# Optimization experiments

Hardware: AMD Instinct MI355X
Metric: run time of the kernel (lower is better)

The kernel has to match this reference:

```python
import jax, jax.numpy as jnp
import numpy as np

EMBD_SIZE = 128
NUM_HEADS = 8
HEAD_SIZE = 16

def setup_inputs() -> dict:
    key = jax.random.key(0)
    ks = jax.random.split(key, 6)
    B, S = 8, 2048
    x = jax.random.normal(ks[0], (B, S, EMBD_SIZE), dtype=jnp.float32)
    # per-head Linear weights, torch layout [out, in] stacked over heads -> [H, hs, E]
    sc = 1.0 / np.sqrt(EMBD_SIZE)
    Wk = jax.random.normal(ks[1], (NUM_HEADS, HEAD_SIZE, EMBD_SIZE), dtype=jnp.float32) * sc
    Wq = jax.random.normal(ks[2], (NUM_HEADS, HEAD_SIZE, EMBD_SIZE), dtype=jnp.float32) * sc
    Wv = jax.random.normal(ks[3], (NUM_HEADS, HEAD_SIZE, EMBD_SIZE), dtype=jnp.float32) * sc
    Wp = jax.random.normal(ks[4], (EMBD_SIZE, NUM_HEADS * HEAD_SIZE), dtype=jnp.float32) * sc
    bp = jax.random.normal(ks[5], (EMBD_SIZE,), dtype=jnp.float32) * 0.01
    return {"x": x, "Wk": Wk, "Wq": Wq, "Wv": Wv, "Wp": Wp, "bp": bp}

def reference(x, Wk, Wq, Wv, Wp, bp):
    # x: [B,S,E]; W{k,q,v}: [H,hs,E]; Wp: [E,H*hs]
    B, S, E = x.shape
    H, hs, _ = Wk.shape
    q = jnp.einsum('bse,hde->bhsd', x, Wq)
    k = jnp.einsum('bse,hde->bhsd', x, Wk)
    v = jnp.einsum('bse,hde->bhsd', x, Wv)
    # NOTE: original code MULTIPLIES by sqrt(head_size) (k.shape[-1]**0.5)
    scores = jnp.einsum('bhsd,bhtd->bhst', q, k) * (hs ** 0.5)
    wei = jax.nn.softmax(scores, axis=-1)  # dropout is identity in eval mode
    out = jnp.einsum('bhst,bhtd->bhsd', wei, v)
    # concat heads along last dim: [B,S,H*hs]
    out = out.transpose(0, 2, 1, 3).reshape(B, S, H * hs)
    return out @ Wp.T + bp
```

## Files before the change

### kernel.cpp

```cpp
#include <hip/hip_runtime.h>
#include <hip/hip_bf16.h>

constexpr int Bb  = 8;
constexpr int Ss  = 2048;
constexpr int Ee  = 128;
constexpr int Hh  = 8;
constexpr int HSs = 16;
constexpr int QKVSZ = Bb * Hh * Ss * HSs;

typedef _Float16 f16;
typedef __attribute__((ext_vector_type(8)))  _Float16 f16x8;
typedef __attribute__((ext_vector_type(16))) float f32x16;

constexpr float QSCALE = 5.770780163555854f;

__device__ __forceinline__ unsigned pack_rtz(float lo, float hi) {
    union { __fp16 __attribute__((ext_vector_type(2))) h; unsigned u; } c;
    c.h = __builtin_amdgcn_cvt_pkrtz(lo, hi);
    return c.u;
}
__device__ __forceinline__ unsigned pack_rne(float lo, float hi) {
    union { __attribute__((ext_vector_type(2))) _Float16 h; unsigned u; } c;
    c.h[0] = (f16)lo; c.h[1] = (f16)hi;
    return c.u;
}

__global__ __launch_bounds__(256) void prep_w(
    const float* __restrict__ Wq, const float* __restrict__ Wk,
    const float* __restrict__ Wv, const float* __restrict__ Wp,
    f16* __restrict__ wh)
{
    int i = (blockIdx.x * 256 + threadIdx.x) * 4;
    const float* src = (i < 16384) ? (Wq + i)
                     : (i < 32768) ? (Wk + i - 16384)
                     : (i < 49152) ? (Wv + i - 32768) : (Wp + i - 49152);
    float4 v = *(const float4*)src;
    union { f16 h[4]; uint2 u; } c;
    c.h[0] = (f16)v.x; c.h[1] = (f16)v.y; c.h[2] = (f16)v.z; c.h[3] = (f16)v.w;
    *(uint2*)(wh + i) = c.u;
}

__global__ __launch_bounds__(256) void qkv_kernel(
    const float* __restrict__ x, const f16* __restrict__ wh,
    f16* __restrict__ qo, f16* __restrict__ ko, f16* __restrict__ vo)
{
    constexpr int LDW = 136;
    __shared__ __align__(16) f16 Xs[32 * LDW];

    const int mat = blockIdx.y;
    const int rowbase = blockIdx.x * 32;

    for (int idx = threadIdx.x; idx < 32 * 32; idx += 256) {
        const int r = idx >> 5, cp = idx & 31;
        float4 v = *(const float4*)(x + (size_t)(rowbase + r) * Ee + cp * 4);
        union { f16 h[4]; uint2 u; } c;
        c.h[0] = (f16)v.x; c.h[1] = (f16)v.y; c.h[2] = (f16)v.z; c.h[3] = (f16)v.w;
        *(uint2*)&Xs[r * LDW + cp * 4] = c.u;
    }
    __syncthreads();

    const int wv_ = threadIdx.x >> 6, lane = threadIdx.x & 63;
    const int h = lane >> 5, n31 = lane & 31;

    f16x8 A[8];
#pragma unroll
    for (int t = 0; t < 8; ++t)
        A[t] = *(const f16x8*)&Xs[n31 * LDW + 16 * t + 8 * h];
    __syncthreads();

    const int c = wv_ * 32 + n31;
    const f16* wr = wh + mat * 16384 + (size_t)c * Ee + 8 * h;
    f32x16 acc = {};
#pragma unroll
    for (int t = 0; t < 8; ++t)
        acc = __builtin_amdgcn_mfma_f32_32x32x16_f16(A[t], *(const f16x8*)(wr + 16 * t), acc, 0, 0, 0);

    const float scale = (mat == 1) ? QSCALE : 1.f;
#pragma unroll
    for (int r = 0; r < 16; ++r) {
        const int row = (r & 3) + 8 * (r >> 2) + 4 * h;
        Xs[row * LDW + c] = (f16)(acc[r] * scale);
    }
    __syncthreads();

    f16* dst = (mat == 0) ? qo : ((mat == 1) ? ko : vo);
    const int b = rowbase >> 11;
    const int s0 = rowbase & 2047;
    if (mat < 2) {
        for (int i = threadIdx.x; i < 512; i += 256) {
            const int head = i >> 6, rem = i & 63;
            const int s = rem >> 1, dh = rem & 1;
            const int bh = b * Hh + head;
            *(uint4*)(dst + ((size_t)bh * Ss + s0 + s) * HSs + dh * 8) =
                *(const uint4*)&Xs[s * LDW + head * HSs + dh * 8];
        }
    } else {
        for (int i = threadIdx.x; i < 512; i += 256) {
            const int head = i >> 6, rem = i & 63;
            const int d = rem & 15, ehalf = (rem >> 4) & 1, squart = rem >> 5;
            const int bh = b * Hh + head;
            union { f16 hv[8]; uint4 u; } pkt;
#pragma unroll
            for (int j = 0; j < 8; ++j) {
                const int ls = squart * 16 + ehalf * 8 + j;
                pkt.hv[j] = Xs[ls * LDW + head * HSs + d];
            }
            const size_t go = (size_t)bh * 32768 + (s0 >> 6) * 1024
                            + ((((s0 & 32) >> 4)) + squart) * 256 + ehalf * 128 + d * 8;
            *(uint4*)(dst + go) = pkt.u;
        }
    }
}

__device__ __forceinline__ void cb_exchange(const unsigned* pw, int h,
                                            f16x8& Blo, f16x8& Bhi) {
    unsigned exa = (unsigned)__shfl_xor((int)(h ? pw[0] : pw[2]), 32, 64);
    unsigned exb = (unsigned)__shfl_xor((int)(h ? pw[1] : pw[3]), 32, 64);
    unsigned exc = (unsigned)__shfl_xor((int)(h ? pw[4] : pw[6]), 32, 64);
    unsigned exd = (unsigned)__shfl_xor((int)(h ? pw[5] : pw[7]), 32, 64);
    union { unsigned u[4]; f16x8 v; } B1, B2;
    if (h == 0) {
        B1.u[0] = pw[0]; B1.u[1] = pw[1]; B1.u[2] = exa; B1.u[3] = exb;
        B2.u[0] = pw[4]; B2.u[1] = pw[5]; B2.u[2] = exc; B2.u[3] = exd;
    } else {
        B1.u[0] = exa; B1.u[1] = exb; B1.u[2] = pw[2]; B1.u[3] = pw[3];
        B2.u[0] = exc; B2.u[1] = exd; B2.u[2] = pw[6]; B2.u[3] = pw[7];
    }
    Blo = B1.v; Bhi = B2.v;
}

__global__ __launch_bounds__(256) void attn_kernel(
    const f16* __restrict__ qg, const f16* __restrict__ kg,
    const f16* __restrict__ vg, f16* __restrict__ og)
{
    __shared__ __align__(16) f16 Ks[2][64 * 24];
    __shared__ __align__(16) f16 Vf[2][2048];

    const int blk  = blockIdx.x;
    const int w_   = blk >> 3;
    const int bh   = (blk & 7) * 8 + (w_ >> 4);
    const int qblk = w_ & 15;
    const int wv_  = threadIdx.x >> 6;
    const int lane = threadIdx.x & 63;
    const int h    = lane >> 5;
    const int q31  = lane & 31;
    const int qbase = qblk * 128 + wv_ * 32;

    {
        const int i = threadIdx.x;
        const int bb = i >> 7, rem = i & 127;
        const int g = rem >> 5, hh = (rem >> 4) & 1, sub = rem & 15;
        const unsigned one2 = 0x3C003C00u;
        uint4 val = (sub == 0) ? (uint4){one2, one2, one2, one2} : (uint4){0, 0, 0, 0};
        *(uint4*)&Vf[bb][g * 512 + hh * 256 + 128 + sub * 8] = val;
    }

    const f16x8 qf = *(const f16x8*)(qg + ((size_t)bh * Ss + qbase + q31) * HSs + 8 * h);

    const bool isK = threadIdx.x < 128;
    const int  i   = threadIdx.x & 127;
    const f16* gsrc = isK ? (kg + (size_t)bh * Ss * HSs + i * 8)
                          : (vg + (size_t)bh * 32768 + i * 8);
    const int koff = (i >> 1) * 24 + (i & 1) * 8;
    const int voff = (i >> 5) * 512 + ((i >> 4) & 1) * 256 + (i & 15) * 8;
    f16x8 sreg = *(const f16x8*)gsrc;

    if (isK) *(f16x8*)&Ks[0][koff] = sreg; else *(f16x8*)&Vf[0][voff] = sreg;
    gsrc += 1024; sreg = *(const f16x8*)gsrc;

    f32x16 acc = {};
    const f32x16 z16 = {};
    float m = -1e30f;

    for (int it = 0; it < Ss / 64; ++it) {
        __syncthreads();
        if (it < Ss / 64 - 1) {
            const int nb = (it + 1) & 1;
            if (isK) *(f16x8*)&Ks[nb][koff] = sreg; else *(f16x8*)&Vf[nb][voff] = sreg;
            gsrc += 1024; sreg = *(const f16x8*)gsrc;
        }
        const int cb = it & 1;

        f16x8 ka0 = *(const f16x8*)&Ks[cb][q31 * 24 + 8 * h];
        f16x8 ka1 = *(const f16x8*)&Ks[cb][(32 + q31) * 24 + 8 * h];
        f32x16 st0 = __builtin_amdgcn_mfma_f32_32x32x16_f16(ka0, qf, z16, 0, 0, 0);
        f32x16 st1 = __builtin_amdgcn_mfma_f32_32x32x16_f16(ka1, qf, z16, 0, 0, 0);

        float mx = st0[0];
#pragma unroll
        for (int t = 1; t < 16; ++t) mx = fmaxf(mx, st0[t]);
#pragma unroll
        for (int t = 0; t < 16; ++t) mx = fmaxf(mx, st1[t]);
        mx = fmaxf(mx, __shfl_xor(mx, 32, 64));
        const float mnew = fmaxf(m, mx);
        const float corr = __builtin_amdgcn_exp2f(m - mnew);
#pragma unroll
        for (int r = 0; r < 9; ++r) acc[r] *= corr;
        m = mnew;

#pragma unroll
        for (int t = 0; t < 16; ++t) st0[t] = __builtin_amdgcn_exp2f(st0[t] - mnew);
#pragma unroll
        for (int t = 0; t < 16; ++t) st1[t] = __builtin_amdgcn_exp2f(st1[t] - mnew);
        unsigned pw0[8], pw1[8];
#pragma unroll
        for (int r = 0; r < 8; ++r) pw0[r] = pack_rtz(st0[2 * r], st0[2 * r + 1]);
#pragma unroll
        for (int r = 0; r < 8; ++r) pw1[r] = pack_rtz(st1[2 * r], st1[2 * r + 1]);
        f16x8 B1, B2, B3, B4;
        cb_exchange(pw0, h, B1, B2);
        cb_exchange(pw1, h, B3, B4);

        f16x8 va0 = *(const f16x8*)&Vf[cb][0 * 512 + lane * 8];
        f16x8 va1 = *(const f16x8*)&Vf[cb][1 * 512 + lane * 8];
        f16x8 va2 = *(const f16x8*)&Vf[cb][2 * 512 + lane * 8];
        f16x8 va3 = *(const f16x8*)&Vf[cb][3 * 512 + lane * 8];
        acc = __builtin_amdgcn_mfma_f32_32x32x16_f16(va0, B1, acc, 0, 0, 0);
        acc = __builtin_amdgcn_mfma_f32_32x32x16_f16(va1, B2, acc, 0, 0, 0);
        acc = __builtin_amdgcn_mfma_f32_32x32x16_f16(va2, B3, acc, 0, 0, 0);
        acc = __builtin_amdgcn_mfma_f32_32x32x16_f16(va3, B4, acc, 0, 0, 0);
    }

    const float l = acc[8] + __shfl_xor(acc[8], 32, 64);
    const float inv = 1.f / l;
    const int b = bh >> 3, head = bh & 7;
    f16* op = og + ((size_t)b * Ss + qbase + q31) * Ee + head * HSs;
    uint2 lo = { pack_rne(acc[0] * inv, acc[1] * inv), pack_rne(acc[2] * inv, acc[3] * inv) };
    uint2 hi = { pack_rne(acc[4] * inv, acc[5] * inv), pack_rne(acc[6] * inv, acc[7] * inv) };
    *(uint2*)(op + 4 * h)     = lo;
    *(uint2*)(op + 8 + 4 * h) = hi;
}

__global__ __launch_bounds__(256) void proj_kernel(
    const f16* __restrict__ oh, const f16* __restrict__ wph,
    const float* __restrict__ bp, float* __restrict__ out)
{
    constexpr int LDW = 136;
    __shared__ __align__(16) f16 Os[32 * LDW];
    const int rowbase = blockIdx.x * 32;

    for (int idx = threadIdx.x; idx < 512; idx += 256) {
        const int r = idx >> 4, cp = idx & 15;
        *(f16x8*)&Os[r * LDW + cp * 8] =
            *(const f16x8*)(oh + (size_t)(rowbase + r) * Ee + cp * 8);
    }
    __syncthreads();

    const int wv_ = threadIdx.x >> 6, lane = threadIdx.x & 63;
    const int h = lane >> 5, n31 = lane & 31;

    f16x8 A[8];
#pragma unroll
    for (int t = 0; t < 8; ++t)
        A[t] = *(const f16x8*)&Os[n31 * LDW + 16 * t + 8 * h];

    const int e = wv_ * 32 + n31;
    const f16* wr = wph + (size_t)e * Ee + 8 * h;
    f32x16 acc = {};
#pragma unroll
    for (int t = 0; t < 8; ++t)
        acc = __builtin_amdgcn_mfma_f32_32x32x16_f16(A[t], *(const f16x8*)(wr + 16 * t), acc, 0, 0, 0);

    const float bias = bp[e];
#pragma unroll
    for (int r = 0; r < 16; ++r) {
        const int R = rowbase + (r & 3) + 8 * (r >> 2) + 4 * h;
        out[(size_t)R * Ee + e] = acc[r] + bias;
    }
}

extern "C" void kernel_launch(void* const* d_in, const int* in_sizes, int n_in,
                              void* d_out, int out_size, void* d_ws, size_t ws_size,
                              hipStream_t stream)
{
    const float* x  = (const float*)d_in[0];
    const float* Wk = (const float*)d_in[1];
    const float* Wq = (const float*)d_in[2];
    const float* Wv = (const float*)d_in[3];
    const float* Wp = (const float*)d_in[4];
    const float* bp = (const float*)d_in[5];
    float* out = (float*)d_out;

    f16* ws = (f16*)d_ws;
    f16* qh = ws;
    f16* kh = ws + (size_t)QKVSZ;
    f16* vh = ws + (size_t)2 * QKVSZ;
    f16* oh = ws + (size_t)3 * QKVSZ;
    f16* wh = ws + (size_t)4 * QKVSZ;

    prep_w<<<64, 256, 0, stream>>>(Wq, Wk, Wv, Wp, wh);
    qkv_kernel<<<dim3(Bb * Ss / 32, 3), 256, 0, stream>>>(x, wh, qh, kh, vh);
    attn_kernel<<<Bb * Hh * (Ss / 128), 256, 0, stream>>>(qh, kh, vh, oh);
    proj_kernel<<<Bb * Ss / 32, 256, 0, stream>>>(oh, wh + 49152, bp, out);
}
```

Measured before the change: 145.0 us.

## Drop LDS staging in attention; load K/V fragments directly from global

The attention kernel changes from 256-thread blocks that share K/V tiles through double-buffered LDS to single-wavefront blocks that load their MFMA fragments straight from global memory into registers, prefetching the next tile. This removes the per-iteration __syncthreads and the LDS round trips. To make this possible, the QKV kernel now writes V in a pre-swizzled fragment layout that includes the ones/zero padding used for the row-sum column, which doubles the V buffer, and it writes Q/K directly from registers instead of staging through shared memory. In exchange, each wavefront reads K/V from global or L2 on its own, with no reuse across the four waves that used to share a tile.

After: 137.6 us. -5.1%, faster.

```diff
diff --git a/kernel.cpp b/kernel.cpp
--- a/kernel.cpp
+++ b/kernel.cpp
@@ -66,7 +66,6 @@
 #pragma unroll
     for (int t = 0; t < 8; ++t)
         A[t] = *(const f16x8*)&Xs[n31 * LDW + 16 * t + 8 * h];
-    __syncthreads();
 
     const int c = wv_ * 32 + n31;
     const f16* wr = wh + mat * 16384 + (size_t)c * Ee + 8 * h;
@@ -75,39 +74,37 @@
     for (int t = 0; t < 8; ++t)
         acc = __builtin_amdgcn_mfma_f32_32x32x16_f16(A[t], *(const f16x8*)(wr + 16 * t), acc, 0, 0, 0);
 
-    const float scale = (mat == 1) ? QSCALE : 1.f;
-#pragma unroll
-    for (int r = 0; r < 16; ++r) {
-        const int row = (r & 3) + 8 * (r >> 2) + 4 * h;
-        Xs[row * LDW + c] = (f16)(acc[r] * scale);
-    }
-    __syncthreads();
-
-    f16* dst = (mat == 0) ? qo : ((mat == 1) ? ko : vo);
     const int b = rowbase >> 11;
     const int s0 = rowbase & 2047;
+    const int head = c >> 4, d = c & 15;
+    const int bh = b * Hh + head;
+
     if (mat < 2) {
+        f16* dst = (mat == 0) ? qo : ko;
+        const float scale = (mat == 1) ? QSCALE : 1.f;
+#pragma unroll
+        for (int r = 0; r < 16; ++r) {
+            const int s = s0 + (r & 3) + 8 * (r >> 2) + 4 * h;
+            dst[((size_t)bh * Ss + s) * HSs + d] = (f16)(acc[r] * scale);
+        }
+    } else {
+        const int it = s0 >> 6, g0 = (s0 >> 4) & 3;
+        f16* vb = vo + (size_t)bh * 65536 + it * 2048;
+#pragma unroll
+        for (int rq = 0; rq < 4; ++rq) {
+            union { f16 hv[4]; uint2 u; } pk4;
+#pragma unroll
+            for (int i = 0; i < 4; ++i) pk4.hv[i] = (f16)acc[4 * rq + i];
+            *(uint2*)(vb + (g0 + (rq >> 1)) * 512 + (d + 32 * (rq & 1)) * 8 + 4 * h) = pk4.u;
+        }
         for (int i = threadIdx.x; i < 512; i += 256) {
-            const int head = i >> 6, rem = i & 63;
-            const int s = rem >> 1, dh = rem & 1;
-            const int bh = b * Hh + head;
-            *(uint4*)(dst + ((size_t)bh * Ss + s0 + s) * HSs + dh * 8) =
-                *(const uint4*)&Xs[s * LDW + head * HSs + dh * 8];
-        }
-    } else {
-        for (int i = threadIdx.x; i < 512; i += 256) {
-            const int head = i >> 6, rem = i & 63;
-            const int d = rem & 15, ehalf = (rem >> 4) & 1, squart = rem >> 5;
-            const int bh = b * Hh + head;
-            union { f16 hv[8]; uint4 u; } pkt;
-#pragma unroll
-            for (int j = 0; j < 8; ++j) {
-                const int ls = squart * 16 + ehalf * 8 + j;
-                pkt.hv[j] = Xs[ls * LDW + head * HSs + d];
-            }
-            const size_t go = (size_t)bh * 32768 + (s0 >> 6) * 1024
-                            + ((((s0 & 32) >> 4)) + squart) * 256 + ehalf * 128 + d * 8;
-            *(uint4*)(dst + go) = pkt.u;
+            const int gp = i >> 8, hd = (i >> 5) & 7, cc = i & 31;
+            const int lanep = (cc < 16) ? 16 + cc : 32 + cc;
+            const unsigned one2 = 0x3C003C00u;
+            uint4 val = ((cc & 15) == 0) ? (uint4){one2, one2, one2, one2}
+                                         : (uint4){0, 0, 0, 0};
+            *(uint4*)(vo + (size_t)(b * Hh + hd) * 65536 + it * 2048
+                      + (g0 + gp) * 512 + lanep * 8) = val;
         }
     }
 }
@@ -129,60 +126,46 @@
     Blo = B1.v; Bhi = B2.v;
 }
 
-__global__ __launch_bounds__(256) void attn_kernel(
+__global__ __launch_bounds__(64, 4) void attn_kernel(
     const f16* __restrict__ qg, const f16* __restrict__ kg,
     const f16* __restrict__ vg, f16* __restrict__ og)
 {
-    __shared__ __align__(16) f16 Ks[2][64 * 24];
-    __shared__ __align__(16) f16 Vf[2][2048];
-
     const int blk  = blockIdx.x;
-    const int w_   = blk >> 3;
-    const int bh   = (blk & 7) * 8 + (w_ >> 4);
-    const int qblk = w_ & 15;
-    const int wv_  = threadIdx.x >> 6;
-    const int lane = threadIdx.x & 63;
+    const int bh   = (blk & 7) * 8 + (blk >> 9);
+    const int qblk = (blk >> 3) & 63;
+    const int lane = threadIdx.x;
     const int h    = lane >> 5;
     const int q31  = lane & 31;
-    const int qbase = qblk * 128 + wv_ * 32;
-
-    {
-        const int i = threadIdx.x;
-        const int bb = i >> 7, rem = i & 127;
-        const int g = rem >> 5, hh = (rem >> 4) & 1, sub = rem & 15;
-        const unsigned one2 = 0x3C003C00u;
-        uint4 val = (sub == 0) ? (uint4){one2, one2, one2, one2} : (uint4){0, 0, 0, 0};
-        *(uint4*)&Vf[bb][g * 512 + hh * 256 + 128 + sub * 8] = val;
-    }
+    const int qbase = qblk * 32;
 
     const f16x8 qf = *(const f16x8*)(qg + ((size_t)bh * Ss + qbase + q31) * HSs + 8 * h);
 
-    const bool isK = threadIdx.x < 128;
-    const int  i   = threadIdx.x & 127;
-    const f16* gsrc = isK ? (kg + (size_t)bh * Ss * HSs + i * 8)
-                          : (vg + (size_t)bh * 32768 + i * 8);
-    const int koff = (i >> 1) * 24 + (i & 1) * 8;
-    const int voff = (i >> 5) * 512 + ((i >> 4) & 1) * 256 + (i & 15) * 8;
-    f16x8 sreg = *(const f16x8*)gsrc;
-
-    if (isK) *(f16x8*)&Ks[0][koff] = sreg; else *(f16x8*)&Vf[0][voff] = sreg;
-    gsrc += 1024; sreg = *(const f16x8*)gsrc;
+    const f16* pk = kg + (size_t)bh * Ss * HSs + q31 * 16 + 8 * h;
+    const f16* pv = vg + (size_t)bh * 65536 + lane * 8;
+
+    f16x8 ka0 = *(const f16x8*)pk;
+    f16x8 ka1 = *(const f16x8*)(pk + 512);
+    f16x8 va0 = *(const f16x8*)(pv);
+    f16x8 va1 = *(const f16x8*)(pv + 512);
+    f16x8 va2 = *(const f16x8*)(pv + 1024);
+    f16x8 va3 = *(const f16x8*)(pv + 1536);
 
     f32x16 acc = {};
     const f32x16 z16 = {};
     float m = -1e30f;
 
     for (int it = 0; it < Ss / 64; ++it) {
-        __syncthreads();
+        f16x8 nk0, nk1, nv0, nv1, nv2, nv3;
         if (it < Ss / 64 - 1) {
-            const int nb = (it + 1) & 1;
-            if (isK) *(f16x8*)&Ks[nb][koff] = sreg; else *(f16x8*)&Vf[nb][voff] = sreg;
-            gsrc += 1024; sreg = *(const f16x8*)gsrc;
-        }
-        const int cb = it & 1;
-
-        f16x8 ka0 = *(const f16x8*)&Ks[cb][q31 * 24 + 8 * h];
-        f16x8 ka1 = *(const f16x8*)&Ks[cb][(32 + q31) * 24 + 8 * h];
+            pk += 1024; pv += 2048;
+            nk0 = *(const f16x8*)pk;
+            nk1 = *(const f16x8*)(pk + 512);
+            nv0 = *(const f16x8*)(pv);
+            nv1 = *(const f16x8*)(pv + 512);
+            nv2 = *(const f16x8*)(pv + 1024);
+            nv3 = *(const f16x8*)(pv + 1536);
+        }
+
         f32x16 st0 = __builtin_amdgcn_mfma_f32_32x32x16_f16(ka0, qf, z16, 0, 0, 0);
         f32x16 st1 = __builtin_amdgcn_mfma_f32_32x32x16_f16(ka1, qf, z16, 0, 0, 0);
 
@@ -211,14 +194,13 @@
         cb_exchange(pw0, h, B1, B2);
         cb_exchange(pw1, h, B3, B4);
 
-        f16x8 va0 = *(const f16x8*)&Vf[cb][0 * 512 + lane * 8];
-        f16x8 va1 = *(const f16x8*)&Vf[cb][1 * 512 + lane * 8];
-        f16x8 va2 = *(const f16x8*)&Vf[cb][2 * 512 + lane * 8];
-        f16x8 va3 = *(const f16x8*)&Vf[cb][3 * 512 + lane * 8];
         acc = __builtin_amdgcn_mfma_f32_32x32x16_f16(va0, B1, acc, 0, 0, 0);
         acc = __builtin_amdgcn_mfma_f32_32x32x16_f16(va1, B2, acc, 0, 0, 0);
         acc = __builtin_amdgcn_mfma_f32_32x32x16_f16(va2, B3, acc, 0, 0, 0);
         acc = __builtin_amdgcn_mfma_f32_32x32x16_f16(va3, B4, acc, 0, 0, 0);
+
+        ka0 = nk0; ka1 = nk1;
+        va0 = nv0; va1 = nv1; va2 = nv2; va3 = nv3;
     }
 
     const float l = acc[8] + __shfl_xor(acc[8], 32, 64);
@@ -285,11 +267,11 @@
     f16* qh = ws;
     f16* kh = ws + (size_t)QKVSZ;
     f16* vh = ws + (size_t)2 * QKVSZ;
-    f16* oh = ws + (size_t)3 * QKVSZ;
-    f16* wh = ws + (size_t)4 * QKVSZ;
+    f16* oh = ws + (size_t)4 * QKVSZ;
+    f16* wh = ws + (size_t)5 * QKVSZ;
 
     prep_w<<<64, 256, 0, stream>>>(Wq, Wk, Wv, Wp, wh);
     qkv_kernel<<<dim3(Bb * Ss / 32, 3), 256, 0, stream>>>(x, wh, qh, kh, vh);
-    attn_kernel<<<Bb * Hh * (Ss / 128), 256, 0, stream>>>(qh, kh, vh, oh);
+    attn_kernel<<<Bb * Hh * (Ss / 32), 64, 0, stream>>>(qh, kh, vh, oh);
     proj_kernel<<<Bb * Ss / 32, 256, 0, stream>>>(oh, wh + 49152, bp, out);
 }
```
